# Performance work log

Hardware: AMD Instinct MI355X
Metric: run time of the kernel (lower is better)

The kernel has to match this reference:

```python
import jax, jax.numpy as jnp
import numpy as np

GAMMA = 0.99


def setup_inputs() -> dict:
    key = jax.random.key(0)
    ks = jax.random.split(key, 6)
    T, D, H = 65536, 1024, 1024
    s1 = 1.0 / np.sqrt(D)
    s2 = 1.0 / np.sqrt(H)
    return {
        "rewards": jax.random.normal(ks[0], (T,), jnp.float32),
        "obs": jax.random.normal(ks[1], (T, D), jnp.float32),
        "W1": jax.random.normal(ks[2], (D, H), jnp.float32) * s1,
        "b1": jnp.zeros((H,), jnp.float32),
        "W2": jax.random.normal(ks[3], (H, H), jnp.float32) * s2,
        "b2": jnp.zeros((H,), jnp.float32),
        "W3": jax.random.normal(ks[4], (H, 1), jnp.float32) * s2,
        "b3": jnp.zeros((1,), jnp.float32),
    }


def _discounted_returns(rewards):
    # G[i] = r[i] + gamma * G[i+1], computed as a reverse scan
    def step(g, r):
        g = r + GAMMA * g
        return g, g
    _, G = jax.lax.scan(step, jnp.zeros((), rewards.dtype), rewards, reverse=True)
    return G


def reference(rewards, obs, W1, b1, W2, b2, W3, b3):
    G = _discounted_returns(rewards)              # [T]
    h = jax.nn.relu(obs @ W1 + b1)                # [T, H]
    h = jax.nn.relu(h @ W2 + b2)                  # [T, H]
    V = (h @ W3 + b3).reshape(-1)                 # [T]
    return G - V
```

## Files before the change

kernel.cpp:

```cpp
#include <hip/hip_runtime.h>

typedef __bf16 bf16x8 __attribute__((ext_vector_type(8)));
typedef __bf16 bf16x4 __attribute__((ext_vector_type(4)));
typedef float  f32x4  __attribute__((ext_vector_type(4)));

#define GAMMA 0.99f

__device__ __forceinline__ void gload_lds16(const void* g, void* l) {
  __builtin_amdgcn_global_load_lds(
      (const __attribute__((address_space(1))) void*)g,
      (__attribute__((address_space(3))) void*)l, 16, 0, 0);
}

#define VMCNT(n) asm volatile("s_waitcnt vmcnt(" #n ")" ::: "memory")
#define BAR() __builtin_amdgcn_s_barrier()
#define MFMA(d, a, b) d = __builtin_amdgcn_mfma_f32_16x16x32_bf16(a, b, d, 0, 0, 0)

__global__ __launch_bounds__(1024) void mega_prep(
    const float* __restrict__ rw, float* __restrict__ G,
    const float* __restrict__ obs, __bf16* __restrict__ obsb,
    const float* __restrict__ W1, const float* __restrict__ W2,
    __bf16* __restrict__ BT1, __bf16* __restrict__ BT2) {
  __shared__ float smem[4224];
  const int blk = blockIdx.x;
  const int t = threadIdx.x;
  if (blk == 0) {
    float* sv = smem;
    const float4* rp = (const float4*)(rw + t * 64);
    float4 lv[16];
#pragma unroll
    for (int i = 0; i < 16; ++i) lv[i] = rp[i];
    float loc[64];
#pragma unroll
    for (int i = 0; i < 16; ++i) {
      loc[4 * i + 0] = lv[i].x; loc[4 * i + 1] = lv[i].y;
      loc[4 * i + 2] = lv[i].z; loc[4 * i + 3] = lv[i].w;
    }
    float g = 0.f;
#pragma unroll
    for (int j = 63; j >= 0; --j) { g = loc[j] + GAMMA * g; loc[j] = g; }
    sv[t] = g;
    float W = GAMMA;
#pragma unroll
    for (int i = 0; i < 6; ++i) W *= W;
    float v = g;
    for (int s = 1; s < 1024; s <<= 1) {
      __syncthreads();
      float o = (t + s < 1024) ? sv[t + s] : 0.f;
      __syncthreads();
      v += W * o;
      sv[t] = v;
      W *= W;
    }
    __syncthreads();
    const float nxt = (t < 1023) ? sv[t + 1] : 0.f;
    float pw = GAMMA;
#pragma unroll
    for (int j = 63; j >= 0; --j) {
      G[t * 64 + j] = loc[j] + pw * nxt;
      pw *= GAMMA;
    }
  } else if (blk <= 2048) {
    const size_t base = (size_t)(blk - 1) * 32768 + (size_t)t * 8;
#pragma unroll
    for (int it = 0; it < 4; ++it) {
      const size_t e = base + (size_t)it * 8192;
      const f32x4* p = (const f32x4*)(obs + e);
      f32x4 u0 = __builtin_nontemporal_load(p);
      f32x4 u1 = __builtin_nontemporal_load(p + 1);
      bf16x8 o = {(__bf16)u0[0], (__bf16)u0[1], (__bf16)u0[2], (__bf16)u0[3],
                  (__bf16)u1[0], (__bf16)u1[1], (__bf16)u1[2], (__bf16)u1[3]};
      *(bf16x8*)(obsb + e) = o;
    }
  } else {
    const int sub = t >> 8, tt = t & 255;
    const int wi = (blk - 2049) * 4 + sub;
    const float* W = (wi >= 1024) ? W2 : W1;
    __bf16* O = (wi >= 1024) ? BT2 : BT1;
    const int tile = wi & 1023;
    const int ti = tile >> 5, tj = tile & 31;
    float* s = smem + sub * 1056;
    const int rr = tt >> 3, c4 = (tt & 7) * 4;
    float4 v = *(const float4*)(W + (size_t)(ti * 32 + rr) * 1024 + tj * 32 + c4);
    s[rr * 33 + c4 + 0] = v.x; s[rr * 33 + c4 + 1] = v.y;
    s[rr * 33 + c4 + 2] = v.z; s[rr * 33 + c4 + 3] = v.w;
    __syncthreads();
    bf16x4 o = {(__bf16)s[(c4 + 0) * 33 + rr], (__bf16)s[(c4 + 1) * 33 + rr],
                (__bf16)s[(c4 + 2) * 33 + rr], (__bf16)s[(c4 + 3) * 33 + rr]};
    *(bf16x4*)(O + (size_t)(tj * 32 + rr) * 1024 + ti * 32 + c4) = o;
  }
}

#define GEMM_KLOOP(APTR, BPTR)                                                 \
  extern __shared__ char lds[];                                                \
  const int t = threadIdx.x, lane = t & 63, w = t >> 6;                        \
  const int wsr = w >> 2, wsc = w & 3, g = lane >> 4, l15 = lane & 15;         \
  const int bid = blockIdx.x;                                                  \
  const int mb = (bid & 7) * 32 + ((bid >> 3) >> 2);                           \
  const int nb = (bid >> 3) & 3;                                               \
  const size_t stg_off =                                                       \
      (size_t)(t >> 2) * 2048 + (size_t)(((t & 3) ^ ((t >> 3) & 3)) * 16);     \
  const char* Ag = (const char*)(APTR) + (size_t)mb * 524288 + stg_off;        \
  const char* Bg = (const char*)(BPTR) + (size_t)nb * 524288 + stg_off;        \
  const int csw = (g ^ ((l15 >> 1) & 3)) << 4;                                 \
  const int arb = (wsr * 64 + l15) * 64 + csw;                                 \
  const int brb = (wsc * 32 + l15) * 64 + csw + 16384;                         \
  f32x4 acc[2][4][2][2];                                                       \
  const f32x4 zero = {0.f, 0.f, 0.f, 0.f};                                     \
  _Pragma("unroll") for (int a_ = 0; a_ < 2; ++a_)                             \
  _Pragma("unroll") for (int b_ = 0; b_ < 4; ++b_)                             \
  _Pragma("unroll") for (int c_ = 0; c_ < 2; ++c_)                             \
  _Pragma("unroll") for (int d_ = 0; d_ < 2; ++d_)                             \
    acc[a_][b_][c_][d_] = zero;                                                \
  auto STA = [&](int buf, int kt) {                                            \
    const char* s = Ag + kt * 64;                                              \
    char* d = lds + buf * 32768 + t * 16;                                      \
    gload_lds16(s, d);                                                         \
    gload_lds16(s + 262144, d + 8192);                                         \
  };                                                                           \
  auto STB = [&](int buf, int kt) {                                            \
    const char* s = Bg + kt * 64;                                              \
    char* d = lds + buf * 32768 + 16384 + t * 16;                              \
    gload_lds16(s, d);                                                         \
    gload_lds16(s + 262144, d + 8192);                                         \
  };                                                                           \
  auto COMPUTE = [&](int bc) {                                                 \
    const char* ab = lds + bc * 32768;                                         \
    bf16x8 bfr[2][2], afr[4];                                                  \
    _Pragma("unroll") for (int nh = 0; nh < 2; ++nh)                           \
    _Pragma("unroll") for (int j = 0; j < 2; ++j)                              \
      bfr[nh][j] = *(const bf16x8*)(ab + brb + (nh * 128 + j * 16) * 64);      \
    _Pragma("unroll") for (int i = 0; i < 4; ++i)                              \
      afr[i] = *(const bf16x8*)(ab + arb + (i * 16) * 64);                     \
    __builtin_amdgcn_s_setprio(1);                                             \
    _Pragma("unroll") for (int i = 0; i < 4; ++i)                              \
    _Pragma("unroll") for (int nh = 0; nh < 2; ++nh)                           \
    _Pragma("unroll") for (int j = 0; j < 2; ++j)                              \
      MFMA(acc[0][i][nh][j], bfr[nh][j], afr[i]);                              \
    __builtin_amdgcn_s_setprio(0);                                             \
    _Pragma("unroll") for (int i = 0; i < 4; ++i)                              \
      afr[i] = *(const bf16x8*)(ab + arb + ((128 + i * 16) * 64));             \
    __builtin_amdgcn_s_setprio(1);                                             \
    _Pragma("unroll") for (int i = 0; i < 4; ++i)                              \
    _Pragma("unroll") for (int nh = 0; nh < 2; ++nh)                           \
    _Pragma("unroll") for (int j = 0; j < 2; ++j)                              \
      MFMA(acc[1][i][nh][j], bfr[nh][j], afr[i]);                              \
    __builtin_amdgcn_s_setprio(0);                                             \
  };                                                                           \
  STA(0, 0); STB(0, 0);                                                        \
  STA(1, 1); STB(1, 1);                                                        \
  STA(2, 2); STB(2, 2);                                                        \
  int bc = 0;                                                                  \
  for (int kt = 0; kt < 29; ++kt) {                                            \
    int bs = bc + 3; if (bs >= 4) bs -= 4;                                     \
    STA(bs, kt + 3);                                                           \
    STB(bs, kt + 3);                                                           \
    VMCNT(12);                                                                 \
    BAR();                                                                     \
    COMPUTE(bc);                                                               \
    BAR();                                                                     \
    bc = (bc + 1) & 3;                                                         \
  }                                                                            \
  VMCNT(8);                                                                    \
  BAR();                                                                       \
  COMPUTE(bc);                                                                 \
  BAR();                                                                       \
  bc = (bc + 1) & 3;                                                           \
  VMCNT(4);                                                                    \
  BAR();                                                                       \
  COMPUTE(bc);                                                                 \
  BAR();                                                                       \
  bc = (bc + 1) & 3;                                                           \
  VMCNT(0);                                                                    \
  BAR();                                                                       \
  COMPUTE(bc);

__global__ __launch_bounds__(512, 2) void gemm1(
    const __bf16* __restrict__ obsb, const __bf16* __restrict__ BT1,
    const float* __restrict__ b1, __bf16* __restrict__ h1) {
  GEMM_KLOOP(obsb, BT1)
  f32x4 b1q[2][2];
#pragma unroll
  for (int nh = 0; nh < 2; ++nh)
#pragma unroll
    for (int j = 0; j < 2; ++j)
      b1q[nh][j] =
          *(const f32x4*)(b1 + nb * 256 + nh * 128 + wsc * 32 + j * 16 + g * 4);
#pragma unroll
  for (int mh = 0; mh < 2; ++mh)
#pragma unroll
    for (int i = 0; i < 4; ++i) {
      const size_t mrow = (size_t)(mb * 256 + mh * 128 + wsr * 64 + i * 16 + l15);
#pragma unroll
      for (int nh = 0; nh < 2; ++nh)
#pragma unroll
        for (int j = 0; j < 2; ++j) {
          f32x4 v = acc[mh][i][nh][j];
          v.x += b1q[nh][j].x; v.y += b1q[nh][j].y;
          v.z += b1q[nh][j].z; v.w += b1q[nh][j].w;
          v.x = v.x > 0.f ? v.x : 0.f;
          v.y = v.y > 0.f ? v.y : 0.f;
          v.z = v.z > 0.f ? v.z : 0.f;
          v.w = v.w > 0.f ? v.w : 0.f;
          bf16x4 o = {(__bf16)v.x, (__bf16)v.y, (__bf16)v.z, (__bf16)v.w};
          *(bf16x4*)(h1 + mrow * 1024 + nb * 256 + nh * 128 + wsc * 32 +
                     j * 16 + g * 4) = o;
        }
    }
}

__global__ __launch_bounds__(512, 2) void gemm2(
    const __bf16* __restrict__ h1, const __bf16* __restrict__ BT2,
    const float* __restrict__ b2, const float* __restrict__ W3,
    float* __restrict__ V4) {
  GEMM_KLOOP(h1, BT2)
  f32x4 b2q[2][2], w3q[2][2];
#pragma unroll
  for (int nh = 0; nh < 2; ++nh)
#pragma unroll
    for (int j = 0; j < 2; ++j) {
      const int C = nb * 256 + nh * 128 + wsc * 32 + j * 16 + g * 4;
      b2q[nh][j] = *(const f32x4*)(b2 + C);
      w3q[nh][j] = *(const f32x4*)(W3 + C);
    }
  float p[2][4];
#pragma unroll
  for (int mh = 0; mh < 2; ++mh)
#pragma unroll
    for (int i = 0; i < 4; ++i) {
      float s = 0.f;
#pragma unroll
      for (int nh = 0; nh < 2; ++nh)
#pragma unroll
        for (int j = 0; j < 2; ++j) {
          f32x4 v = acc[mh][i][nh][j];
          v.x += b2q[nh][j].x; v.y += b2q[nh][j].y;
          v.z += b2q[nh][j].z; v.w += b2q[nh][j].w;
          v.x = v.x > 0.f ? v.x : 0.f;
          v.y = v.y > 0.f ? v.y : 0.f;
          v.z = v.z > 0.f ? v.z : 0.f;
          v.w = v.w > 0.f ? v.w : 0.f;
          s += v.x * w3q[nh][j].x + v.y * w3q[nh][j].y +
               v.z * w3q[nh][j].z + v.w * w3q[nh][j].w;
        }
      p[mh][i] = s;
    }
#pragma unroll
  for (int mh = 0; mh < 2; ++mh)
#pragma unroll
    for (int i = 0; i < 4; ++i) {
      p[mh][i] += __shfl_xor(p[mh][i], 16, 64);
      p[mh][i] += __shfl_xor(p[mh][i], 32, 64);
    }
  float* vp = (float*)lds;
  if (g == 0) {
#pragma unroll
    for (int mh = 0; mh < 2; ++mh)
#pragma unroll
      for (int i = 0; i < 4; ++i)
        vp[wsc * 256 + mh * 128 + wsr * 64 + i * 16 + l15] = p[mh][i];
  }
  __syncthreads();
  if (t < 256) {
    float s = vp[t] + vp[256 + t] + vp[512 + t] + vp[768 + t];
    V4[(size_t)nb * 65536 + mb * 256 + t] = s;
  }
}

__global__ __launch_bounds__(256) void final_kernel(const float* __restrict__ G,
                                                    const float* __restrict__ V4,
                                                    const float* __restrict__ b3,
                                                    float* __restrict__ out) {
  int i = blockIdx.x * 256 + threadIdx.x;
  out[i] = G[i] - (V4[i] + V4[65536 + i] + V4[131072 + i] + V4[196608 + i] + b3[0]);
}

extern "C" void kernel_launch(void* const* d_in, const int* in_sizes, int n_in,
                              void* d_out, int out_size, void* d_ws, size_t ws_size,
                              hipStream_t stream) {
  const float* rewards = (const float*)d_in[0];
  const float* obs = (const float*)d_in[1];
  const float* W1 = (const float*)d_in[2];
  const float* b1 = (const float*)d_in[3];
  const float* W2 = (const float*)d_in[4];
  const float* b2 = (const float*)d_in[5];
  const float* W3 = (const float*)d_in[6];
  const float* b3 = (const float*)d_in[7];
  float* out = (float*)d_out;

  char* ws = (char*)d_ws;
  __bf16* BT1 = (__bf16*)(ws);
  __bf16* BT2 = (__bf16*)(ws + (2u << 20));
  float* V4 = (float*)(ws + (4u << 20));
  float* G = (float*)(ws + (5u << 20));
  __bf16* obsb = (__bf16*)(ws + (8u << 20));
  __bf16* h1 = (__bf16*)(ws + (136u << 20));

  hipFuncSetAttribute((const void*)gemm1,
                      hipFuncAttributeMaxDynamicSharedMemorySize, 131072);
  hipFuncSetAttribute((const void*)gemm2,
                      hipFuncAttributeMaxDynamicSharedMemorySize, 131072);

  mega_prep<<<2561, 1024, 0, stream>>>(rewards, G, obs, obsb, W1, W2, BT1, BT2);
  gemm1<<<1024, 512, 131072, stream>>>(obsb, BT1, b1, h1);
  gemm2<<<1024, 512, 131072, stream>>>(h1, BT2, b2, W3, V4);
  final_kernel<<<256, 256, 0, stream>>>(G, V4, b3, out);
}
```

Measured before the change: 340.1 us.

## Split obs conversion and GEMMs into four row chunks for cache locality

The obs fp32->bf16 conversion moves out of the prep kernel into its own kernel. The pipeline now runs as four sequential chunks of 16K rows (conv, gemm1, gemm2), each GEMM taking a row-block base offset. The aim is to keep each chunk's bf16 obs and h1 intermediates resident in the last-level cache between stages instead of streaming the full 128MB buffers through HBM. In exchange there are more kernel launches, and each GEMM launch has only 256 blocks, which may leave CUs underused and add tail effects.

Measured after the change: 382.8 us. +12.5%, slower.

```diff
diff --git a/kernel.cpp b/kernel.cpp
--- a/kernel.cpp
+++ b/kernel.cpp
@@ -16,9 +16,8 @@
 #define BAR() __builtin_amdgcn_s_barrier()
 #define MFMA(d, a, b) d = __builtin_amdgcn_mfma_f32_16x16x32_bf16(a, b, d, 0, 0, 0)
 
-__global__ __launch_bounds__(1024) void mega_prep(
+__global__ __launch_bounds__(1024) void prep(
     const float* __restrict__ rw, float* __restrict__ G,
-    const float* __restrict__ obs, __bf16* __restrict__ obsb,
     const float* __restrict__ W1, const float* __restrict__ W2,
     __bf16* __restrict__ BT1, __bf16* __restrict__ BT2) {
   __shared__ float smem[4224];
@@ -60,21 +59,9 @@
       G[t * 64 + j] = loc[j] + pw * nxt;
       pw *= GAMMA;
     }
-  } else if (blk <= 2048) {
-    const size_t base = (size_t)(blk - 1) * 32768 + (size_t)t * 8;
-#pragma unroll
-    for (int it = 0; it < 4; ++it) {
-      const size_t e = base + (size_t)it * 8192;
-      const f32x4* p = (const f32x4*)(obs + e);
-      f32x4 u0 = __builtin_nontemporal_load(p);
-      f32x4 u1 = __builtin_nontemporal_load(p + 1);
-      bf16x8 o = {(__bf16)u0[0], (__bf16)u0[1], (__bf16)u0[2], (__bf16)u0[3],
-                  (__bf16)u1[0], (__bf16)u1[1], (__bf16)u1[2], (__bf16)u1[3]};
-      *(bf16x8*)(obsb + e) = o;
-    }
   } else {
     const int sub = t >> 8, tt = t & 255;
-    const int wi = (blk - 2049) * 4 + sub;
+    const int wi = (blk - 1) * 4 + sub;
     const float* W = (wi >= 1024) ? W2 : W1;
     __bf16* O = (wi >= 1024) ? BT2 : BT1;
     const int tile = wi & 1023;
@@ -91,12 +78,27 @@
   }
 }
 
-#define GEMM_KLOOP(APTR, BPTR)                                                 \
+__global__ __launch_bounds__(1024) void conv(const float* __restrict__ obs,
+                                             __bf16* __restrict__ obsb) {
+  const size_t base = (size_t)blockIdx.x * 32768 + (size_t)threadIdx.x * 8;
+#pragma unroll
+  for (int it = 0; it < 4; ++it) {
+    const size_t e = base + (size_t)it * 8192;
+    const f32x4* p = (const f32x4*)(obs + e);
+    f32x4 u0 = __builtin_nontemporal_load(p);
+    f32x4 u1 = __builtin_nontemporal_load(p + 1);
+    bf16x8 o = {(__bf16)u0[0], (__bf16)u0[1], (__bf16)u0[2], (__bf16)u0[3],
+                (__bf16)u1[0], (__bf16)u1[1], (__bf16)u1[2], (__bf16)u1[3]};
+    *(bf16x8*)(obsb + e) = o;
+  }
+}
+
+#define GEMM_PRELUDE(APTR, BPTR)                                               \
   extern __shared__ char lds[];                                                \
   const int t = threadIdx.x, lane = t & 63, w = t >> 6;                        \
   const int wsr = w >> 2, wsc = w & 3, g = lane >> 4, l15 = lane & 15;         \
   const int bid = blockIdx.x;                                                  \
-  const int mb = (bid & 7) * 32 + ((bid >> 3) >> 2);                           \
+  const int mb = mbase + (bid & 7) * 8 + (bid >> 5);                           \
   const int nb = (bid >> 3) & 3;                                               \
   const size_t stg_off =                                                       \
       (size_t)(t >> 2) * 2048 + (size_t)(((t & 3) ^ ((t >> 3) & 3)) * 16);     \
@@ -146,7 +148,9 @@
     _Pragma("unroll") for (int j = 0; j < 2; ++j)                              \
       MFMA(acc[1][i][nh][j], bfr[nh][j], afr[i]);                              \
     __builtin_amdgcn_s_setprio(0);                                             \
-  };                                                                           \
+  };
+
+#define KLOOP_D3()                                                             \
   STA(0, 0); STB(0, 0);                                                        \
   STA(1, 1); STB(1, 1);                                                        \
   STA(2, 2); STB(2, 2);                                                        \
@@ -161,24 +165,15 @@
     BAR();                                                                     \
     bc = (bc + 1) & 3;                                                         \
   }                                                                            \
-  VMCNT(8);                                                                    \
-  BAR();                                                                       \
-  COMPUTE(bc);                                                                 \
-  BAR();                                                                       \
-  bc = (bc + 1) & 3;                                                           \
-  VMCNT(4);                                                                    \
-  BAR();                                                                       \
-  COMPUTE(bc);                                                                 \
-  BAR();                                                                       \
-  bc = (bc + 1) & 3;                                                           \
-  VMCNT(0);                                                                    \
-  BAR();                                                                       \
-  COMPUTE(bc);
+  VMCNT(8);  BAR(); COMPUTE(bc); BAR(); bc = (bc + 1) & 3;                     \
+  VMCNT(4);  BAR(); COMPUTE(bc); BAR(); bc = (bc + 1) & 3;                     \
+  VMCNT(0);  BAR(); COMPUTE(bc);
 
 __global__ __launch_bounds__(512, 2) void gemm1(
     const __bf16* __restrict__ obsb, const __bf16* __restrict__ BT1,
-    const float* __restrict__ b1, __bf16* __restrict__ h1) {
-  GEMM_KLOOP(obsb, BT1)
+    const float* __restrict__ b1, __bf16* __restrict__ h1, int mbase) {
+  GEMM_PRELUDE(obsb, BT1)
+  KLOOP_D3()
   f32x4 b1q[2][2];
 #pragma unroll
   for (int nh = 0; nh < 2; ++nh)
@@ -212,8 +207,9 @@
 __global__ __launch_bounds__(512, 2) void gemm2(
     const __bf16* __restrict__ h1, const __bf16* __restrict__ BT2,
     const float* __restrict__ b2, const float* __restrict__ W3,
-    float* __restrict__ V4) {
-  GEMM_KLOOP(h1, BT2)
+    float* __restrict__ V4, int mbase) {
+  GEMM_PRELUDE(h1, BT2)
+  KLOOP_D3()
   f32x4 b2q[2][2], w3q[2][2];
 #pragma unroll
   for (int nh = 0; nh < 2; ++nh)
@@ -296,13 +292,17 @@
   __bf16* obsb = (__bf16*)(ws + (8u << 20));
   __bf16* h1 = (__bf16*)(ws + (136u << 20));
 
-  hipFuncSetAttribute((const void*)gemm1,
-                      hipFuncAttributeMaxDynamicSharedMemorySize, 131072);
-  hipFuncSetAttribute((const void*)gemm2,
-                      hipFuncAttributeMaxDynamicSharedMemorySize, 131072);
-
-  mega_prep<<<2561, 1024, 0, stream>>>(rewards, G, obs, obsb, W1, W2, BT1, BT2);
-  gemm1<<<1024, 512, 131072, stream>>>(obsb, BT1, b1, h1);
-  gemm2<<<1024, 512, 131072, stream>>>(h1, BT2, b2, W3, V4);
+  (void)hipFuncSetAttribute((const void*)gemm1,
+                            hipFuncAttributeMaxDynamicSharedMemorySize, 131072);
+  (void)hipFuncSetAttribute((const void*)gemm2,
+                            hipFuncAttributeMaxDynamicSharedMemorySize, 131072);
+
+  prep<<<513, 1024, 0, stream>>>(rewards, G, W1, W2, BT1, BT2);
+  for (int c = 0; c < 4; ++c) {
+    const size_t eoff = (size_t)c * 16777216;
+    conv<<<512, 1024, 0, stream>>>(obs + eoff, obsb + eoff);
+    gemm1<<<256, 512, 131072, stream>>>(obsb, BT1, b1, h1, c * 64);
+    gemm2<<<256, 512, 131072, stream>>>(h1, BT2, b2, W3, V4, c * 64);
+  }
   final_kernel<<<256, 256, 0, stream>>>(G, V4, b3, out);
 }
```
